# Kernel tuning notes

Hardware: AMD Instinct MI355X
Metric: run time of the kernel (lower is better)

The kernel has to match this reference:

```python
import jax, jax.numpy as jnp
import numpy as np

STRIDES = (8, 16, 32, 64, 128)
NUM_CLASSES = 80
TOPK = 1000
CONF_THRESH = 0.05
NMS_THRESH = 0.6
IMG_H = IMG_W = 2048
CLASS_OFFSET = 100000.0  # > any box coordinate, makes different-class boxes disjoint


def _level_decode(cls, reg, ctn, scale, stride):
    # cls: [1,C,H,W], reg: [1,4,H,W], ctn: [1,1,H,W]
    C, H, W = cls.shape[1], cls.shape[2], cls.shape[3]
    cls = jnp.transpose(cls[0], (1, 2, 0)).reshape(-1, C)       # [HW, C]
    reg = jnp.transpose(reg[0], (1, 2, 0)).reshape(-1, 4)       # [HW, 4]
    reg = jax.nn.relu(reg * scale) * stride                      # Scale + relu + stride
    ctn = jnp.transpose(ctn[0], (1, 2, 0)).reshape(-1, 1)       # [HW, 1]
    prob = jnp.sqrt(jax.nn.sigmoid(cls) * jax.nn.sigmoid(ctn))  # [HW, C]
    scores = prob.max(axis=-1)
    labels = prob.argmax(axis=-1)
    ys, xs = jnp.meshgrid(jnp.arange(H), jnp.arange(W), indexing='ij')
    anchors = (jnp.stack([xs, ys], axis=-1).reshape(-1, 2).astype(cls.dtype) + 0.5) * stride
    if scores.shape[0] > TOPK:
        scores, idx = jax.lax.top_k(scores, TOPK)
        labels, reg, anchors = labels[idx], reg[idx], anchors[idx]
    # decode (l,t,r,b) deltas around anchor centers -> (x1,y1,x2,y2)
    boxes = jnp.concatenate([anchors - reg[:, :2], anchors + reg[:, 2:]], axis=-1)
    return scores, labels, boxes


def _nms_keep(boxes, scores, valid, thresh):
    # Sequential greedy NMS, same math as the numpy loop in RTEFCOS.nms.
    order = jnp.argsort(-jnp.where(valid, scores, -jnp.inf))
    b = boxes[order]
    v = valid[order]
    x1, y1, x2, y2 = b[:, 0], b[:, 1], b[:, 2], b[:, 3]
    areas = (x2 - x1) * (y2 - y1)
    n = b.shape[0]
    pos = jnp.arange(n)

    def body(i, keep):
        xx1 = jnp.maximum(x1[i], x1)
        yy1 = jnp.maximum(y1[i], y1)
        xx2 = jnp.minimum(x2[i], x2)
        yy2 = jnp.minimum(y2[i], y2)
        inter = jnp.maximum(1e-10, xx2 - xx1) * jnp.maximum(1e-10, yy2 - yy1)
        ovr = inter / (areas[i] + areas - inter + 1e-14)
        suppress = (ovr > thresh) & (pos > i) & keep[i]
        return keep & (~suppress)

    keep_sorted = jax.lax.fori_loop(0, n, body, v)
    return jnp.zeros(n, dtype=bool).at[order].set(keep_sorted)


def reference(cls0, reg0, ctn0, cls1, reg1, ctn1, cls2, reg2, ctn2,
              cls3, reg3, ctn3, cls4, reg4, ctn4, scales):
    levels = [(cls0, reg0, ctn0), (cls1, reg1, ctn1), (cls2, reg2, ctn2),
              (cls3, reg3, ctn3), (cls4, reg4, ctn4)]
    all_s, all_l, all_b = [], [], []
    for lv, (c, r, t) in enumerate(levels):
        s, l, b = _level_decode(c, r, t, scales[lv], STRIDES[lv])
        all_s.append(s); all_l.append(l); all_b.append(b)
    scores = jnp.concatenate(all_s)   # [M]
    labels = jnp.concatenate(all_l)   # [M]
    bboxes = jnp.concatenate(all_b)   # [M, 4]
    valid = scores >= CONF_THRESH     # conf filter as mask (static shapes)
    # class-wise NMS via coordinate-offset trick: boxes of different classes
    # never overlap, so one greedy pass == per-class greedy passes.
    boxes_off = bboxes + labels[:, None].astype(bboxes.dtype) * CLASS_OFFSET
    keep = _nms_keep(boxes_off, scores, valid, NMS_THRESH)
    bboxes = bboxes / jnp.array([IMG_W, IMG_H, IMG_W, IMG_H], dtype=bboxes.dtype)
    bboxes = jnp.clip(bboxes, 0.0, 1.0)
    return bboxes, scores, labels, keep


def setup_inputs():
    key = jax.random.key(0)
    ks = jax.random.split(key, len(STRIDES))
    inp = {}
    for lv, stride in enumerate(STRIDES):
        H = IMG_H // stride
        W = IMG_W // stride
        k1, k2, k3 = jax.random.split(ks[lv], 3)
        inp[f"cls{lv}"] = jax.random.normal(k1, (1, NUM_CLASSES, H, W), jnp.float32)
        inp[f"reg{lv}"] = jax.random.uniform(k2, (1, 4, H, W), jnp.float32)
        inp[f"ctn{lv}"] = jax.random.normal(k3, (1, 1, H, W), jnp.float32)
    inp["scales"] = jnp.ones((5,), jnp.float32)
    return inp
```

## Files before the change

kernel.cpp:

```cpp
#include <hip/hip_runtime.h>
#include <math.h>

#define TOTAL_ANCHORS 87296
#define NTOPK 87040
#define NSEL 4256
#define NWORDS 67
#define NPAD   4288
#define MAXROUNDS 4300
#define CANDMAX 8192
#define NBIN 32768

__device__ __forceinline__ float sigmoidf_(float x) {
    return 1.0f / (1.0f + expf(-x));
}
__device__ __forceinline__ unsigned int f2s(float f) {
    unsigned int u = __float_as_uint(f);
    return u ^ ((u >> 31) ? 0xFFFFFFFFu : 0x80000000u);
}
__device__ __forceinline__ float s2f(unsigned int k) {
    unsigned int u = (k & 0x80000000u) ? (k ^ 0x80000000u) : ~k;
    return __uint_as_float(u);
}
__device__ __forceinline__ void level_of(int g, int& lv, int& base, int& W, int& stride) {
    if (g < 65536)      { lv = 0; base = 0;     W = 256; stride = 8;   }
    else if (g < 81920) { lv = 1; base = 65536; W = 128; stride = 16;  }
    else if (g < 86016) { lv = 2; base = 81920; W = 64;  stride = 32;  }
    else if (g < 87040) { lv = 3; base = 86016; W = 32;  stride = 64;  }
    else                { lv = 4; base = 87040; W = 16;  stride = 128; }
}

struct InPtrs {
    const float* cls[5];
    const float* reg[5];
    const float* ctn[5];
    const float* scales;
};

__global__ __launch_bounds__(256) void cmax_kernel(InPtrs in,
        unsigned long long* __restrict__ cmax) {
    int a = blockIdx.x * 256 + threadIdx.x;
    int cg = blockIdx.y;
    int lv, base, W, stride;
    level_of(a, lv, base, W, stride);
    (void)stride;
    int p = a - base;
    int HW = W * W;
    const float* cls = in.cls[lv];
    float sctn = sigmoidf_(in.ctn[lv][p]);
    int c0 = cg * 8;
    float v[8];
    #pragma unroll
    for (int k = 0; k < 8; ++k) v[k] = cls[(c0 + k) * HW + p];
    unsigned long long best = 0ull;
    #pragma unroll
    for (int k = 0; k < 8; ++k) {
        float pr = sqrtf(__fmul_rn(sigmoidf_(v[k]), sctn));
        unsigned long long key = ((unsigned long long)f2s(pr) << 32)
                               | (unsigned long long)(255 - (c0 + k));
        best = (key > best) ? key : best;
    }
    atomicMax(&cmax[a], best);
}

__global__ __launch_bounds__(256) void decode2_kernel(InPtrs in,
        const unsigned long long* __restrict__ cmax,
        unsigned long long* __restrict__ keys, float* __restrict__ scores,
        int* __restrict__ labels, float4* __restrict__ boxes) {
    int g = blockIdx.x * 256 + threadIdx.x;
    int lv, base, W, stride;
    level_of(g, lv, base, W, stride);
    int p = g - base;
    int HW = W * W;
    int x = p & (W - 1);
    int y = p / W;
    unsigned long long mk = cmax[g];
    float best = s2f((unsigned int)(mk >> 32));
    int lbl = 255 - (int)(mk & 0xFFull);
    float scale = in.scales[lv];
    float fs = (float)stride;
    const float* rg = in.reg[lv];
    float r0 = __fmul_rn(fmaxf(__fmul_rn(rg[0 * HW + p], scale), 0.0f), fs);
    float r1 = __fmul_rn(fmaxf(__fmul_rn(rg[1 * HW + p], scale), 0.0f), fs);
    float r2 = __fmul_rn(fmaxf(__fmul_rn(rg[2 * HW + p], scale), 0.0f), fs);
    float r3 = __fmul_rn(fmaxf(__fmul_rn(rg[3 * HW + p], scale), 0.0f), fs);
    float ax = __fmul_rn(__fadd_rn((float)x, 0.5f), fs);
    float ay = __fmul_rn(__fadd_rn((float)y, 0.5f), fs);
    float4 b;
    b.x = __fsub_rn(ax, r0);
    b.y = __fsub_rn(ay, r1);
    b.z = __fadd_rn(ax, r2);
    b.w = __fadd_rn(ay, r3);
    scores[g] = best;
    labels[g] = lbl;
    boxes[g]  = b;
    keys[g] = (mk & 0xFFFFFFFF00000000ull)
            | (unsigned long long)(unsigned int)(~(unsigned int)p);
}

__global__ __launch_bounds__(1024) void hist_kernel(
        const unsigned long long* __restrict__ keys,
        unsigned int* __restrict__ slab) {
    __shared__ unsigned int h[NBIN / 2];
    const int starts[5] = {0, 32768, 65536, 81920, 86016};
    const int ends[5]   = {32768, 65536, 81920, 86016, 87040};
    const int tid = threadIdx.x;
    for (int i = tid; i < NBIN / 2; i += 1024) h[i] = 0u;
    __syncthreads();
    const int s = starts[blockIdx.x], e = ends[blockIdx.x];
    for (int i = s + tid; i < e; i += 1024) {
        unsigned int bin = (unsigned int)(keys[i] >> 48) & 0x7FFFu;
        atomicAdd(&h[bin >> 1], 1u << ((bin & 1u) << 4));
    }
    __syncthreads();
    unsigned int* out = slab + blockIdx.x * (NBIN / 2);
    for (int i = tid; i < NBIN / 2; i += 1024) out[i] = h[i];
}

__global__ __launch_bounds__(1024) void select_kernel(
        const unsigned int* __restrict__ slab, unsigned int* __restrict__ thr) {
    const int lvl = blockIdx.x;
    const int slabA[4] = {0, 2, 3, 4};
    const unsigned int* A = slab + slabA[lvl] * (NBIN / 2);
    const unsigned int* B = (lvl == 0) ? slab + (NBIN / 2) : nullptr;
    const int tid = threadIdx.x;
    __shared__ unsigned int csum[1024];
    unsigned int s = 0;
    for (int w = tid * 16; w < tid * 16 + 16; ++w) {
        unsigned int v = A[w];
        s += (v & 0xFFFFu) + (v >> 16);
        if (B) { v = B[w]; s += (v & 0xFFFFu) + (v >> 16); }
    }
    csum[tid] = s;
    __syncthreads();
    for (int off = 1; off < 1024; off <<= 1) {
        unsigned int v = csum[tid] + ((tid + off < 1024) ? csum[tid + off] : 0u);
        __syncthreads();
        csum[tid] = v;
        __syncthreads();
    }
    unsigned int incl = csum[tid];
    unsigned int incl1 = (tid == 1023) ? 0u : csum[tid + 1];
    if (incl >= 1000u && incl1 < 1000u) {
        unsigned int running = incl1;
        for (int b = tid * 32 + 31; b >= tid * 32; --b) {
            unsigned int v = A[b >> 1];
            unsigned int c = (v >> ((b & 1) << 4)) & 0xFFFFu;
            if (B) { v = B[b >> 1]; c += (v >> ((b & 1) << 4)) & 0xFFFFu; }
            running += c;
            if (running >= 1000u) { thr[lvl] = (unsigned int)b; break; }
        }
    }
}

__global__ __launch_bounds__(1024) void gather_kernel(
        const unsigned long long* __restrict__ keys,
        const unsigned int* __restrict__ thr,
        unsigned long long* __restrict__ cand, unsigned int* __restrict__ cnt) {
    int g = blockIdx.x * 1024 + threadIdx.x;
    int lvl;
    if (g < 65536)      lvl = 0;
    else if (g < 81920) lvl = 1;
    else if (g < 86016) lvl = 2;
    else                lvl = 3;
    unsigned long long k = keys[g];
    bool pass = (((unsigned int)(k >> 48)) & 0x7FFFu) >= thr[lvl];
    __shared__ unsigned int woff[16];
    __shared__ unsigned int base_;
    const int wave = threadIdx.x >> 6, lane = threadIdx.x & 63;
    unsigned long long m = __ballot(pass);
    if (lane == 0) woff[wave] = (unsigned int)__popcll(m);
    __syncthreads();
    if (threadIdx.x == 0) {
        unsigned int tot = 0;
        #pragma unroll
        for (int w = 0; w < 16; ++w) { unsigned int c = woff[w]; woff[w] = tot; tot += c; }
        base_ = atomicAdd(&cnt[lvl << 5], tot);
    }
    __syncthreads();
    if (pass) {
        unsigned int pos = base_ + woff[wave]
                         + (unsigned int)__popcll(m & ((1ull << lane) - 1ull));
        if (pos < CANDMAX) cand[(lvl << 13) + pos] = k;
    }
}

__global__ __launch_bounds__(1024) void finalsort_kernel(
        const unsigned long long* __restrict__ cand,
        const unsigned int* __restrict__ cnt,
        unsigned long long* __restrict__ sel) {
    const int lvl = blockIdx.x;
    const int tid = threadIdx.x;
    __shared__ unsigned long long sk[CANDMAX];
    int n = (int)cnt[lvl << 5];
    if (n > CANDMAX) n = CANDMAX;
    int P = 1024;
    while (P < n) P <<= 1;
    for (int i = tid; i < P; i += 1024)
        sk[i] = (i < n) ? cand[(lvl << 13) + i] : 0ull;
    __syncthreads();
    for (int kk = 2; kk <= P; kk <<= 1) {
        for (int j = kk >> 1; j > 0; j >>= 1) {
            for (int i = tid; i < P; i += 1024) {
                int ixj = i ^ j;
                if (ixj > i) {
                    unsigned long long a = sk[i], b = sk[ixj];
                    bool sw = ((i & kk) == 0) ? (a < b) : (a > b);
                    if (sw) { sk[i] = b; sk[ixj] = a; }
                }
            }
            __syncthreads();
        }
    }
    if (tid < 1000) sel[lvl * 1000 + tid] = sk[tid];
}

__global__ __launch_bounds__(256) void fin_kernel(
        const unsigned long long* __restrict__ sel,
        const float* __restrict__ scores, const int* __restrict__ labels,
        const float4* __restrict__ boxes, float* __restrict__ out,
        float4* __restrict__ entbox, float* __restrict__ entarea,
        int* __restrict__ entvalid, unsigned long long* __restrict__ ekeyG) {
    int pos = blockIdx.x * 256 + threadIdx.x;
    if (pos >= NSEL) return;
    int g;
    if (pos < 4000) {
        int lv = pos / 1000;
        const int offs_[4] = {0, 65536, 81920, 86016};
        unsigned long long key = sel[pos];
        unsigned int p = ~((unsigned int)(key & 0xFFFFFFFFull));
        g = offs_[lv] + (int)p;
    } else {
        g = 87040 + (pos - 4000);
    }
    float sc = scores[g];
    int lb = labels[g];
    float4 bx = boxes[g];
    const float inv = 1.0f / 2048.0f;
    out[pos * 4 + 0] = fminf(fmaxf(__fmul_rn(bx.x, inv), 0.0f), 1.0f);
    out[pos * 4 + 1] = fminf(fmaxf(__fmul_rn(bx.y, inv), 0.0f), 1.0f);
    out[pos * 4 + 2] = fminf(fmaxf(__fmul_rn(bx.z, inv), 0.0f), 1.0f);
    out[pos * 4 + 3] = fminf(fmaxf(__fmul_rn(bx.w, inv), 0.0f), 1.0f);
    out[17024 + pos] = sc;
    out[21280 + pos] = (float)lb;
    out[25536 + pos] = 0.0f;
    float off = __fmul_rn((float)lb, 100000.0f);
    float4 eb;
    eb.x = __fadd_rn(bx.x, off); eb.y = __fadd_rn(bx.y, off);
    eb.z = __fadd_rn(bx.z, off); eb.w = __fadd_rn(bx.w, off);
    entbox[pos] = eb;
    entarea[pos] = __fmul_rn(__fsub_rn(eb.z, eb.x), __fsub_rn(eb.w, eb.y));
    int valid = (sc >= 0.05f) ? 1 : 0;
    entvalid[pos] = valid;
    float effs = valid ? sc : -INFINITY;
    ekeyG[pos] = ((unsigned long long)f2s(effs) << 32) | (unsigned int)(~(unsigned int)pos);
}

__device__ __forceinline__ int count_greater(const unsigned long long* A, int n,
                                             unsigned long long x) {
    int lo = 0, hi = n;
    while (lo < hi) { int m = (lo + hi) >> 1; if (A[m] > x) lo = m + 1; else hi = m; }
    return lo;
}
__global__ __launch_bounds__(1024) void rank_kernel(
        const unsigned long long* __restrict__ ekeyG,
        const float4* __restrict__ entbox, const float* __restrict__ entarea,
        const int* __restrict__ entvalid,
        int* __restrict__ order, float4* __restrict__ sbox,
        float* __restrict__ sarea, int* __restrict__ svalid) {
    __shared__ unsigned long long eL[4000];
    __shared__ unsigned long long sk4[256];
    const int tid = threadIdx.x;
    for (int i = tid; i < 4000; i += 1024) eL[i] = ekeyG[i];
    if (tid < 256) sk4[tid] = ekeyG[4000 + tid];
    __syncthreads();
    for (int kk = 2; kk <= 256; kk <<= 1) {
        for (int j = kk >> 1; j > 0; j >>= 1) {
            if (tid < 256) {
                int ixj = tid ^ j;
                if (ixj > tid) {
                    unsigned long long a = sk4[tid], b = sk4[ixj];
                    bool sw = ((tid & kk) == 0) ? (a < b) : (a > b);
                    if (sw) { sk4[tid] = b; sk4[ixj] = a; }
                }
            }
            __syncthreads();
        }
    }
    int pos = blockIdx.x * 1024 + tid;
    if (pos < NSEL) {
        unsigned long long x = (pos < 4000) ? eL[pos] : ekeyG[pos];
        int rank = count_greater(eL,        1000, x)
                 + count_greater(eL + 1000, 1000, x)
                 + count_greater(eL + 2000, 1000, x)
                 + count_greater(eL + 3000, 1000, x)
                 + count_greater(sk4,        256, x);
        order[rank]  = pos;
        sbox[rank]   = entbox[pos];
        sarea[rank]  = entarea[pos];
        svalid[rank] = entvalid[pos];
    }
}

__global__ __launch_bounds__(64) void mask_kernel(
        const float4* __restrict__ sbox, const float* __restrict__ sarea,
        const int* __restrict__ svalid,
        unsigned long long* __restrict__ maskC,
        unsigned long long* __restrict__ pend0G,
        unsigned int* __restrict__ pend1G) {
    int colTile = blockIdx.x, rowTile = blockIdx.y;
    if (colTile > rowTile) return;
    __shared__ float4 cb[64];
    __shared__ float ca[64];
    int tid = threadIdx.x;
    int col0 = colTile * 64;
    int c = col0 + tid;
    int vcol = 0;
    if (c < NSEL) { cb[tid] = sbox[c]; ca[tid] = sarea[c]; vcol = svalid[c]; }
    else { cb[tid] = make_float4(0.f, 0.f, 0.f, 0.f); ca[tid] = 0.f; }
    unsigned long long unkw = __ballot(vcol != 0);
    __syncthreads();
    int i = rowTile * 64 + tid;
    unsigned long long bits = 0ull;
    if (i < NSEL) {
        float4 b = sbox[i];
        float ar = sarea[i];
        for (int j = 0; j < 64; ++j) {
            float xx1 = fmaxf(b.x, cb[j].x);
            float yy1 = fmaxf(b.y, cb[j].y);
            float xx2 = fminf(b.z, cb[j].z);
            float yy2 = fminf(b.w, cb[j].w);
            float w = fmaxf(1e-10f, __fsub_rn(xx2, xx1));
            float h = fmaxf(1e-10f, __fsub_rn(yy2, yy1));
            float inter = __fmul_rn(w, h);
            float denom = __fadd_rn(__fsub_rn(__fadd_rn(ar, ca[j]), inter), 1e-14f);
            float ovr = __fdiv_rn(inter, denom);
            if (ovr > 0.6f) bits |= (1ull << j);
        }
    }
    maskC[(size_t)colTile * NPAD + i] = bits;
    if (colTile < rowTile && i < NSEL && (bits & unkw)) {
        if (colTile < 64) atomicOr(&pend0G[i], 1ull << colTile);
        else              atomicOr(&pend1G[i], 1u << (colTile - 64));
    }
}

__global__ __launch_bounds__(1024) void sweep_kernel(
        const unsigned long long* __restrict__ maskC,
        const unsigned long long* __restrict__ pend0G,
        const unsigned int* __restrict__ pend1G,
        const int* __restrict__ order, const int* __restrict__ svalid,
        float* __restrict__ out_keep) {
    const int tid = threadIdx.x;
    const int lane = tid & 63;
    const int wave = tid >> 6;
    __shared__ unsigned long long keptL[NWORDS], unkL[NWORDS];
    __shared__ unsigned long long nk[NWORDS], nkC[NWORDS], ndC[NWORDS];
    __shared__ unsigned long long cm0s;
    __shared__ unsigned int cm1s;
    __shared__ int anych;
    __shared__ int wflag[16];

    unsigned long long md[5], pend0[5];
    unsigned int pendH[5];
    #pragma unroll
    for (int k = 0; k < 5; ++k) {
        int b = wave + 16 * k;
        unsigned long long w = 0ull;
        md[k] = 0ull; pend0[k] = 0ull; pendH[k] = 0u;
        if (b < NWORDS) {
            int c = b * 64 + lane;
            int v = (c < NSEL) ? svalid[c] : 0;
            w = __ballot(v != 0);
            md[k]    = maskC[(size_t)b * NPAD + c];
            pend0[k] = pend0G[c];
            pendH[k] = pend1G[c];
            if (lane == 0) { unkL[b] = w; keptL[b] = 0ull; nk[b] = 0ull; }
        }
    }
    if (tid == 0) { cm0s = 0ull; cm1s = 0u; }
    __syncthreads();

    for (int round = 0; round < MAXROUNDS; ++round) {
        unsigned long long cm0 = cm0s;
        unsigned int cm1 = cm1s;
        #pragma unroll
        for (int k = 0; k < 5; ++k) {
            int b = wave + 16 * k;
            bool kp = false, dec = false;
            if (b < NWORDS) {
                int c = b * 64 + lane;
                unsigned long long uw = unkL[b];
                if ((uw >> lane) & 1ull) {
                    bool rem = false;
                    unsigned long long todo = pend0[k] & cm0;
                    while (todo) {
                        int w = __ffsll((long long)todo) - 1;
                        todo &= todo - 1ull;
                        unsigned long long m = maskC[(size_t)w * NPAD + c];
                        if (m & nk[w]) { rem = true; break; }
                        if ((m & unkL[w]) == 0ull) pend0[k] &= ~(1ull << w);
                    }
                    if (!rem) {
                        unsigned int todoH = pendH[k] & cm1;
                        while (todoH) {
                            int bit = __ffs(todoH) - 1;
                            todoH &= todoH - 1u;
                            int w = 64 + bit;
                            unsigned long long m = maskC[(size_t)w * NPAD + c];
                            if (m & nk[w]) { rem = true; break; }
                            if ((m & unkL[w]) == 0ull) pendH[k] &= ~(1u << bit);
                        }
                    }
                    unsigned long long below = (1ull << lane) - 1ull;
                    if (!rem && (md[k] & keptL[b] & below)) rem = true;
                    if (!rem && pend0[k] == 0ull && pendH[k] == 0u
                             && (md[k] & uw & below) == 0ull) kp = true;
                    dec = rem || kp;
                }
            }
            unsigned long long kb = __ballot(kp);
            unsigned long long db = __ballot(dec);
            if (b < NWORDS && lane == 0) { nkC[b] = kb; ndC[b] = db; }
        }
        __syncthreads();
        int any = 0;
        #pragma unroll
        for (int k = 0; k < 5; ++k) {
            int b = wave + 16 * k;
            if (b >= NWORDS) continue;
            unsigned long long db = ndC[b];
            if (lane == 0) {
                keptL[b] |= nkC[b];
                unkL[b]  &= ~db;
                nk[b]     = nkC[b];
            }
            any |= (db != 0ull) ? 1 : 0;
        }
        if (lane == 0) wflag[wave] = any;
        __syncthreads();
        if (tid == 0) {
            unsigned long long c0 = 0ull; unsigned int c1 = 0u; int a = 0;
            for (int w = 0; w < 64; ++w) if (ndC[w]) c0 |= (1ull << w);
            for (int w = 64; w < NWORDS; ++w) if (ndC[w]) c1 |= (1u << (w - 64));
            #pragma unroll
            for (int w = 0; w < 16; ++w) a |= wflag[w];
            cm0s = c0; cm1s = c1; anych = a;
        }
        __syncthreads();
        if (!anych) break;
    }

    #pragma unroll
    for (int k = 0; k < 5; ++k) {
        int b = wave + 16 * k;
        if (b >= NWORDS) continue;
        int c = b * 64 + lane;
        if (c < NSEL && ((keptL[b] >> lane) & 1ull)) out_keep[order[c]] = 1.0f;
    }
}

constexpr size_t OFF_KEYS    = 0;
constexpr size_t OFF_SCORES  = OFF_KEYS    + 698368;
constexpr size_t OFF_LABELS  = OFF_SCORES  + 349184;
constexpr size_t OFF_BOXES   = OFF_LABELS  + 349184;
constexpr size_t OFF_SEL     = OFF_BOXES   + 1396736;
constexpr size_t OFF_ORDER   = OFF_SEL     + 32000;
constexpr size_t OFF_SBOX    = OFF_ORDER   + 17024;
constexpr size_t OFF_SAREA   = OFF_SBOX    + 68096;
constexpr size_t OFF_SVALID  = OFF_SAREA   + 17024;
constexpr size_t OFF_MASK    = OFF_SVALID  + 17024;
constexpr size_t OFF_CMAX    = OFF_MASK    + (size_t)NWORDS * NPAD * 8;
constexpr size_t OFF_CNT     = OFF_CMAX    + 698368;
constexpr size_t OFF_PEND0   = OFF_CNT     + 512;
constexpr size_t OFF_PEND1   = OFF_PEND0   + (size_t)NPAD * 8;
constexpr size_t OFF_THR     = OFF_PEND1   + (size_t)NPAD * 4;
constexpr size_t OFF_SLAB    = OFF_THR     + 64;
constexpr size_t OFF_CAND    = OFF_SLAB    + 5u * 16384u * 4u;
constexpr size_t OFF_EKEY    = OFF_CAND    + 4u * CANDMAX * 8u;
constexpr size_t OFF_ENTBOX  = OFF_EKEY    + 34048;
constexpr size_t OFF_ENTAREA = OFF_ENTBOX  + 68096;
constexpr size_t OFF_ENTVAL  = OFF_ENTAREA + 17024;
constexpr size_t MEMSET_BYTES = 698368 + 512 + (size_t)NPAD * 8 + (size_t)NPAD * 4;

extern "C" void kernel_launch(void* const* d_in, const int* in_sizes, int n_in,
                              void* d_out, int out_size, void* d_ws, size_t ws_size,
                              hipStream_t stream) {
    (void)in_sizes; (void)n_in; (void)out_size; (void)ws_size;
    InPtrs P;
    for (int lv = 0; lv < 5; ++lv) {
        P.cls[lv] = (const float*)d_in[3 * lv + 0];
        P.reg[lv] = (const float*)d_in[3 * lv + 1];
        P.ctn[lv] = (const float*)d_in[3 * lv + 2];
    }
    P.scales = (const float*)d_in[15];

    char* ws = (char*)d_ws;
    unsigned long long* keys   = (unsigned long long*)(ws + OFF_KEYS);
    float*              scores = (float*)             (ws + OFF_SCORES);
    int*                labels = (int*)               (ws + OFF_LABELS);
    float4*             boxes  = (float4*)            (ws + OFF_BOXES);
    unsigned long long* sel    = (unsigned long long*)(ws + OFF_SEL);
    int*                order  = (int*)               (ws + OFF_ORDER);
    float4*             sbox   = (float4*)            (ws + OFF_SBOX);
    float*              sarea  = (float*)             (ws + OFF_SAREA);
    int*                svalid = (int*)               (ws + OFF_SVALID);
    unsigned long long* maskb  = (unsigned long long*)(ws + OFF_MASK);
    unsigned long long* cmax   = (unsigned long long*)(ws + OFF_CMAX);
    unsigned int*       cnt    = (unsigned int*)      (ws + OFF_CNT);
    unsigned long long* pend0  = (unsigned long long*)(ws + OFF_PEND0);
    unsigned int*       pend1  = (unsigned int*)      (ws + OFF_PEND1);
    unsigned int*       thr    = (unsigned int*)      (ws + OFF_THR);
    unsigned int*       slab   = (unsigned int*)      (ws + OFF_SLAB);
    unsigned long long* cand   = (unsigned long long*)(ws + OFF_CAND);
    unsigned long long* ekeyG  = (unsigned long long*)(ws + OFF_EKEY);
    float4*             entbox = (float4*)            (ws + OFF_ENTBOX);
    float*              entarea= (float*)             (ws + OFF_ENTAREA);
    int*                entval = (int*)               (ws + OFF_ENTVAL);
    float* out = (float*)d_out;

    hipMemsetAsync(ws + OFF_CMAX, 0, MEMSET_BYTES, stream);
    cmax_kernel<<<dim3(341, 10), 256, 0, stream>>>(P, cmax);
    decode2_kernel<<<341, 256, 0, stream>>>(P, cmax, keys, scores, labels, boxes);
    hist_kernel<<<5, 1024, 0, stream>>>(keys, slab);
    select_kernel<<<4, 1024, 0, stream>>>(slab, thr);
    gather_kernel<<<85, 1024, 0, stream>>>(keys, thr, cand, cnt);
    finalsort_kernel<<<4, 1024, 0, stream>>>(cand, cnt, sel);
    fin_kernel<<<(NSEL + 255) / 256, 256, 0, stream>>>(sel, scores, labels, boxes, out,
                                                       entbox, entarea, entval, ekeyG);
    rank_kernel<<<(NSEL + 1023) / 1024, 1024, 0, stream>>>(ekeyG, entbox, entarea, entval,
                                                           order, sbox, sarea, svalid);
    mask_kernel<<<dim3(NWORDS, NWORDS), 64, 0, stream>>>(sbox, sarea, svalid,
                                                         maskb, pend0, pend1);
    sweep_kernel<<<1, 1024, 0, stream>>>(maskb, pend0, pend1, order, svalid, out + 25536);
}
```

Before: 131.6 us.

## Drop memset and atomics: per-group cmax buffers, finer histogram slabs, in-kernel zeroing

The per-anchor class max now goes into ten separate per-channel-group buffers that decode2 reduces, replacing the atomicMax into a zeroed buffer. This lets the hipMemsetAsync be removed: select_kernel now zeroes the counters and fin_kernel zeroes the pend buffers. The histogram is split into 8 slabs instead of 5 so more blocks run in parallel, and select sums the matching slabs. In exchange, the cmax traffic grows about tenfold (roughly 7 MB written and then read).

```diff
diff --git a/kernel.cpp b/kernel.cpp
--- a/kernel.cpp
+++ b/kernel.cpp
@@ -9,6 +9,7 @@
 #define MAXROUNDS 4300
 #define CANDMAX 8192
 #define NBIN 32768
+#define NSLAB 8
 
 __device__ __forceinline__ float sigmoidf_(float x) {
     return 1.0f / (1.0f + expf(-x));
@@ -37,7 +38,7 @@
 };
 
 __global__ __launch_bounds__(256) void cmax_kernel(InPtrs in,
-        unsigned long long* __restrict__ cmax) {
+        unsigned long long* __restrict__ cmax2) {
     int a = blockIdx.x * 256 + threadIdx.x;
     int cg = blockIdx.y;
     int lv, base, W, stride;
@@ -59,11 +60,11 @@
                                | (unsigned long long)(255 - (c0 + k));
         best = (key > best) ? key : best;
     }
-    atomicMax(&cmax[a], best);
+    cmax2[(size_t)cg * TOTAL_ANCHORS + a] = best;
 }
 
 __global__ __launch_bounds__(256) void decode2_kernel(InPtrs in,
-        const unsigned long long* __restrict__ cmax,
+        const unsigned long long* __restrict__ cmax2,
         unsigned long long* __restrict__ keys, float* __restrict__ scores,
         int* __restrict__ labels, float4* __restrict__ boxes) {
     int g = blockIdx.x * 256 + threadIdx.x;
@@ -73,7 +74,12 @@
     int HW = W * W;
     int x = p & (W - 1);
     int y = p / W;
-    unsigned long long mk = cmax[g];
+    unsigned long long mk = 0ull;
+    #pragma unroll
+    for (int cg = 0; cg < 10; ++cg) {
+        unsigned long long v = cmax2[(size_t)cg * TOTAL_ANCHORS + g];
+        mk = (v > mk) ? v : mk;
+    }
     float best = s2f((unsigned int)(mk >> 32));
     int lbl = 255 - (int)(mk & 0xFFull);
     float scale = in.scales[lv];
@@ -101,8 +107,8 @@
         const unsigned long long* __restrict__ keys,
         unsigned int* __restrict__ slab) {
     __shared__ unsigned int h[NBIN / 2];
-    const int starts[5] = {0, 32768, 65536, 81920, 86016};
-    const int ends[5]   = {32768, 65536, 81920, 86016, 87040};
+    const int starts[NSLAB] = {0, 16384, 32768, 49152, 65536, 73728, 81920, 86016};
+    const int ends[NSLAB]   = {16384, 32768, 49152, 65536, 73728, 81920, 86016, 87040};
     const int tid = threadIdx.x;
     for (int i = tid; i < NBIN / 2; i += 1024) h[i] = 0u;
     __syncthreads();
@@ -117,18 +123,22 @@
 }
 
 __global__ __launch_bounds__(1024) void select_kernel(
-        const unsigned int* __restrict__ slab, unsigned int* __restrict__ thr) {
+        const unsigned int* __restrict__ slab, unsigned int* __restrict__ thr,
+        unsigned int* __restrict__ cnt) {
     const int lvl = blockIdx.x;
-    const int slabA[4] = {0, 2, 3, 4};
-    const unsigned int* A = slab + slabA[lvl] * (NBIN / 2);
-    const unsigned int* B = (lvl == 0) ? slab + (NBIN / 2) : nullptr;
+    const int slabS[4] = {0, 4, 6, 7};
+    const int slabE[4] = {4, 6, 7, 8};
     const int tid = threadIdx.x;
+    if (lvl == 0 && tid < 128) cnt[tid] = 0u;
     __shared__ unsigned int csum[1024];
     unsigned int s = 0;
-    for (int w = tid * 16; w < tid * 16 + 16; ++w) {
-        unsigned int v = A[w];
-        s += (v & 0xFFFFu) + (v >> 16);
-        if (B) { v = B[w]; s += (v & 0xFFFFu) + (v >> 16); }
+    for (int sb = slabS[lvl]; sb < slabE[lvl]; ++sb) {
+        const unsigned int* A = slab + sb * (NBIN / 2);
+        #pragma unroll 4
+        for (int w = tid * 16; w < tid * 16 + 16; ++w) {
+            unsigned int v = A[w];
+            s += (v & 0xFFFFu) + (v >> 16);
+        }
     }
     csum[tid] = s;
     __syncthreads();
@@ -143,9 +153,11 @@
     if (incl >= 1000u && incl1 < 1000u) {
         unsigned int running = incl1;
         for (int b = tid * 32 + 31; b >= tid * 32; --b) {
-            unsigned int v = A[b >> 1];
-            unsigned int c = (v >> ((b & 1) << 4)) & 0xFFFFu;
-            if (B) { v = B[b >> 1]; c += (v >> ((b & 1) << 4)) & 0xFFFFu; }
+            unsigned int c = 0;
+            for (int sb = slabS[lvl]; sb < slabE[lvl]; ++sb) {
+                unsigned int v = slab[sb * (NBIN / 2) + (b >> 1)];
+                c += (v >> ((b & 1) << 4)) & 0xFFFFu;
+            }
             running += c;
             if (running >= 1000u) { thr[lvl] = (unsigned int)b; break; }
         }
@@ -214,13 +226,16 @@
     if (tid < 1000) sel[lvl * 1000 + tid] = sk[tid];
 }
 
+#define PEND_VEC 3216
 __global__ __launch_bounds__(256) void fin_kernel(
         const unsigned long long* __restrict__ sel,
         const float* __restrict__ scores, const int* __restrict__ labels,
         const float4* __restrict__ boxes, float* __restrict__ out,
         float4* __restrict__ entbox, float* __restrict__ entarea,
-        int* __restrict__ entvalid, unsigned long long* __restrict__ ekeyG) {
+        int* __restrict__ entvalid, unsigned long long* __restrict__ ekeyG,
+        float4* __restrict__ pendzero) {
     int pos = blockIdx.x * 256 + threadIdx.x;
+    if (pos < PEND_VEC) pendzero[pos] = make_float4(0.f, 0.f, 0.f, 0.f);
     if (pos >= NSEL) return;
     int g;
     if (pos < 4000) {
@@ -469,18 +484,17 @@
 constexpr size_t OFF_SAREA   = OFF_SBOX    + 68096;
 constexpr size_t OFF_SVALID  = OFF_SAREA   + 17024;
 constexpr size_t OFF_MASK    = OFF_SVALID  + 17024;
-constexpr size_t OFF_CMAX    = OFF_MASK    + (size_t)NWORDS * NPAD * 8;
-constexpr size_t OFF_CNT     = OFF_CMAX    + 698368;
+constexpr size_t OFF_CMAX2   = OFF_MASK    + (size_t)NWORDS * NPAD * 8;
+constexpr size_t OFF_CNT     = OFF_CMAX2   + 10u * 698368u;
 constexpr size_t OFF_PEND0   = OFF_CNT     + 512;
 constexpr size_t OFF_PEND1   = OFF_PEND0   + (size_t)NPAD * 8;
 constexpr size_t OFF_THR     = OFF_PEND1   + (size_t)NPAD * 4;
 constexpr size_t OFF_SLAB    = OFF_THR     + 64;
-constexpr size_t OFF_CAND    = OFF_SLAB    + 5u * 16384u * 4u;
+constexpr size_t OFF_CAND    = OFF_SLAB    + (size_t)NSLAB * 16384u * 4u;
 constexpr size_t OFF_EKEY    = OFF_CAND    + 4u * CANDMAX * 8u;
 constexpr size_t OFF_ENTBOX  = OFF_EKEY    + 34048;
 constexpr size_t OFF_ENTAREA = OFF_ENTBOX  + 68096;
 constexpr size_t OFF_ENTVAL  = OFF_ENTAREA + 17024;
-constexpr size_t MEMSET_BYTES = 698368 + 512 + (size_t)NPAD * 8 + (size_t)NPAD * 4;
 
 extern "C" void kernel_launch(void* const* d_in, const int* in_sizes, int n_in,
                               void* d_out, int out_size, void* d_ws, size_t ws_size,
@@ -505,7 +519,7 @@
     float*              sarea  = (float*)             (ws + OFF_SAREA);
     int*                svalid = (int*)               (ws + OFF_SVALID);
     unsigned long long* maskb  = (unsigned long long*)(ws + OFF_MASK);
-    unsigned long long* cmax   = (unsigned long long*)(ws + OFF_CMAX);
+    unsigned long long* cmax2  = (unsigned long long*)(ws + OFF_CMAX2);
     unsigned int*       cnt    = (unsigned int*)      (ws + OFF_CNT);
     unsigned long long* pend0  = (unsigned long long*)(ws + OFF_PEND0);
     unsigned int*       pend1  = (unsigned int*)      (ws + OFF_PEND1);
@@ -518,15 +532,15 @@
     int*                entval = (int*)               (ws + OFF_ENTVAL);
     float* out = (float*)d_out;
 
-    hipMemsetAsync(ws + OFF_CMAX, 0, MEMSET_BYTES, stream);
-    cmax_kernel<<<dim3(341, 10), 256, 0, stream>>>(P, cmax);
-    decode2_kernel<<<341, 256, 0, stream>>>(P, cmax, keys, scores, labels, boxes);
-    hist_kernel<<<5, 1024, 0, stream>>>(keys, slab);
-    select_kernel<<<4, 1024, 0, stream>>>(slab, thr);
+    cmax_kernel<<<dim3(341, 10), 256, 0, stream>>>(P, cmax2);
+    decode2_kernel<<<341, 256, 0, stream>>>(P, cmax2, keys, scores, labels, boxes);
+    hist_kernel<<<NSLAB, 1024, 0, stream>>>(keys, slab);
+    select_kernel<<<4, 1024, 0, stream>>>(slab, thr, cnt);
     gather_kernel<<<85, 1024, 0, stream>>>(keys, thr, cand, cnt);
     finalsort_kernel<<<4, 1024, 0, stream>>>(cand, cnt, sel);
     fin_kernel<<<(NSEL + 255) / 256, 256, 0, stream>>>(sel, scores, labels, boxes, out,
-                                                       entbox, entarea, entval, ekeyG);
+                                                       entbox, entarea, entval, ekeyG,
+                                                       (float4*)(ws + OFF_PEND0));
     rank_kernel<<<(NSEL + 1023) / 1024, 1024, 0, stream>>>(ekeyG, entbox, entarea, entval,
                                                            order, sbox, sarea, svalid);
     mask_kernel<<<dim3(NWORDS, NWORDS), 64, 0, stream>>>(sbox, sarea, svalid,
```

After: 120.8 us. -8.2%, faster.
